# Kernel optimization log

Measured on AMD Instinct MI355X. Metric: run time of the kernel, lower is better.

Reference implementation:

```python
import jax, jax.numpy as jnp
import numpy as np

EMBED_DIM = 1024
NUM_HEADS = 16
HEAD_DIM = EMBED_DIM // NUM_HEADS
B, S = 2, 2048


def setup_inputs() -> dict:
    key = jax.random.key(0)
    ks = jax.random.split(key, 12)
    sd = 1.0 / np.sqrt(EMBED_DIM)
    def lin(kw, kb):
        W = jax.random.uniform(kw, (EMBED_DIM, EMBED_DIM), jnp.float32, -sd, sd)
        b = jax.random.uniform(kb, (EMBED_DIM,), jnp.float32, -sd, sd)
        return W, b
    Wq, bq = lin(ks[0], ks[1])
    Wk, bk = lin(ks[2], ks[3])
    Wv, bv = lin(ks[4], ks[5])
    Wo, bo = lin(ks[6], ks[7])
    q = jax.random.normal(ks[8], (B, S, EMBED_DIM), jnp.float32)
    k = jax.random.normal(ks[9], (B, S, EMBED_DIM), jnp.float32)
    v = jax.random.normal(ks[10], (B, S, EMBED_DIM), jnp.float32)
    # broadcastable causal mask: True = keep (mask==0 positions get -inf)
    attn_mask = jnp.tril(jnp.ones((S, S), jnp.bool_))[None, None]
    return {"q": q, "k": k, "v": v,
            "Wq": Wq, "bq": bq, "Wk": Wk, "bk": bk,
            "Wv": Wv, "bv": bv, "Wo": Wo, "bo": bo,
            "attn_mask": attn_mask}


def reference(q, k, v, Wq, bq, Wk, bk, Wv, bv, Wo, bo, attn_mask):
    bsz, tgt_len, _ = q.shape
    src_len = k.shape[1]
    scale = jnp.sqrt(jnp.float32(HEAD_DIM))
    # projections: PyTorch Linear is x @ W.T + b
    qh = (q @ Wq.T + bq).reshape(bsz, tgt_len, NUM_HEADS, HEAD_DIM).transpose(0, 2, 1, 3)
    kh = (k @ Wk.T + bk).reshape(bsz, src_len, NUM_HEADS, HEAD_DIM).transpose(0, 2, 1, 3)
    vh = (v @ Wv.T + bv).reshape(bsz, src_len, NUM_HEADS, HEAD_DIM).transpose(0, 2, 1, 3)
    # [B,H,T,S] scores
    scores = jnp.einsum('bhtd,bhsd->bhts', qh, kh) / scale
    scores = jnp.where(attn_mask, scores, -jnp.inf)
    attn = jax.nn.softmax(scores, axis=-1)
    out = jnp.einsum('bhts,bhsd->bhtd', attn, vh)  # [B,H,T,D]
    out = out.transpose(0, 2, 1, 3).reshape(bsz, tgt_len, EMBED_DIM)
    return out @ Wo.T + bo
```

## Files before the change

kernel.cpp:

```cpp
#include <hip/hip_runtime.h>
#include <hip/hip_bf16.h>
#include <stdint.h>
#include <stddef.h>

typedef __hip_bfloat16 bf16_t;
typedef __attribute__((ext_vector_type(8))) short short8;
typedef __attribute__((ext_vector_type(4))) short short4v;
typedef __attribute__((ext_vector_type(4))) float floatx4;

#define EMBED 1024
#define NHEAD 16
#define HDIM  64
#define BATCH 2
#define SEQ   2048
#define MTOT  (BATCH*SEQ)
#define NEG_INF (-1e30f)
#define SCALE2 0.18033688011112042f

#define MFMA16(a,b,c) __builtin_amdgcn_mfma_f32_16x16x32_bf16(a,b,c,0,0,0)

static __device__ __forceinline__ short bf16_bits(float x) {
    return __builtin_bit_cast(short, __float2bfloat16(x));
}

static __device__ __forceinline__ float fast_exp2(float x) {
#if __has_builtin(__builtin_amdgcn_exp2f)
    return __builtin_amdgcn_exp2f(x);
#else
    return __expf(x * 0.6931471805599453f);
#endif
}

static __device__ __forceinline__ void async_ld16(const bf16_t* g, short* l) {
    __builtin_amdgcn_global_load_lds(
        (const __attribute__((address_space(1))) void*)g,
        (__attribute__((address_space(3))) void*)l,
        16, 0, 0);
}

static __device__ __forceinline__ void store_out(float* p, float v)  { *p = v; }
static __device__ __forceinline__ void store_out(bf16_t* p, float v) { *p = __float2bfloat16(v); }

__global__ __launch_bounds__(256)
void cvt_all(const float* __restrict__ q, const float* __restrict__ k, const float* __restrict__ v,
             const float* __restrict__ wq, const float* __restrict__ wk,
             const float* __restrict__ wv, const float* __restrict__ wo,
             bf16_t* __restrict__ Qx, bf16_t* __restrict__ Kx, bf16_t* __restrict__ Vx,
             bf16_t* __restrict__ Wqb, bf16_t* __restrict__ Wkb,
             bf16_t* __restrict__ Wvb, bf16_t* __restrict__ Wob)
{
    const float* s; bf16_t* d; int n;
    switch (blockIdx.y) {
        case 0:  s = q;  d = Qx;  n = MTOT * EMBED;  break;
        case 1:  s = k;  d = Kx;  n = MTOT * EMBED;  break;
        case 2:  s = v;  d = Vx;  n = MTOT * EMBED;  break;
        case 3:  s = wq; d = Wqb; n = EMBED * EMBED; break;
        case 4:  s = wk; d = Wkb; n = EMBED * EMBED; break;
        case 5:  s = wv; d = Wvb; n = EMBED * EMBED; break;
        default: s = wo; d = Wob; n = EMBED * EMBED; break;
    }
    const int i4 = (int)blockIdx.x * 256 + (int)threadIdx.x;
    if (i4 * 4 < n) {
        const float4 f = ((const float4*)s)[i4];
        short4v o;
        o[0] = bf16_bits(f.x); o[1] = bf16_bits(f.y);
        o[2] = bf16_bits(f.z); o[3] = bf16_bits(f.w);
        ((short4v*)d)[i4] = o;
    }
}

template <typename OutT, bool VT>
static __device__ __forceinline__ void gemm_tile_128(
    const bf16_t* __restrict__ A, const bf16_t* __restrict__ W,
    const float* __restrict__ bias, OutT* __restrict__ C)
{
    const int N = 1024, K = 1024;
    __shared__ alignas(16) short As[128*32];
    __shared__ alignas(16) short Bs[128*32];

    const int tid  = threadIdx.x;
    const int wave = tid >> 6;
    const int lane = tid & 63;
    const int nbn = N >> 7;
    const int bm = (int)blockIdx.x / nbn;
    const int bn = (int)blockIdx.x % nbn;
    const int m0 = bm << 7, n0 = bn << 7;

    const int wm = ((wave >> 1) & 1) << 6;
    const int wn = (wave & 1) << 6;

    floatx4 acc[4][4] = {};

    const int srow = (wave << 5) + (lane >> 2);
    const int scol = (lane & 3) << 3;
    const bf16_t* gA = A + (size_t)(m0 + srow) * K + scol;
    const bf16_t* gB = W + (size_t)(n0 + srow) * K + scol;
    short* lA0 = &As[(wave << 10)];
    short* lA1 = &As[(wave << 10) + 512];
    short* lB0 = &Bs[(wave << 10)];
    short* lB1 = &Bs[(wave << 10) + 512];

    const int fr = lane & 15;
    const int fk = (lane >> 4) << 3;

    for (int k0 = 0; k0 < K; k0 += 32) {
        __syncthreads();
        async_ld16(gA,                  lA0);
        async_ld16(gA + (size_t)16 * K, lA1);
        async_ld16(gB,                  lB0);
        async_ld16(gB + (size_t)16 * K, lB1);
        gA += 32; gB += 32;
        __syncthreads();

        short8 af[4], bfr[4];
        #pragma unroll
        for (int i = 0; i < 4; ++i)
            af[i] = *(const short8*)&As[(wm + (i << 4) + fr) * 32 + fk];
        #pragma unroll
        for (int j = 0; j < 4; ++j)
            bfr[j] = *(const short8*)&Bs[(wn + (j << 4) + fr) * 32 + fk];
        #pragma unroll
        for (int i = 0; i < 4; ++i)
            #pragma unroll
            for (int j = 0; j < 4; ++j)
                acc[i][j] = MFMA16(af[i], bfr[j], acc[i][j]);
    }

    const int q4 = (lane >> 4) << 2;
    #pragma unroll
    for (int j = 0; j < 4; ++j) {
        const int n = n0 + wn + (j << 4) + fr;
        const float bv = bias[n];
        #pragma unroll
        for (int i = 0; i < 4; ++i) {
            const int mb = m0 + wm + (i << 4) + q4;
            if (VT) {
                const int bb = mb >> 11, ss = mb & 2047;
                short4v pk;
                #pragma unroll
                for (int r = 0; r < 4; ++r)
                    pk[r] = bf16_bits(acc[i][j][r] + bv);
                *(short4v*)((bf16_t*)C + ((size_t)(bb * 1024 + n) << 11) + ss) = pk;
            } else {
                #pragma unroll
                for (int r = 0; r < 4; ++r)
                    store_out(&C[(size_t)(mb + r) * N + n], acc[i][j][r] + bv);
            }
        }
    }
}

__global__ __launch_bounds__(256)
void qkv_proj(const bf16_t* __restrict__ xq, const bf16_t* __restrict__ xk,
              const bf16_t* __restrict__ xv,
              const bf16_t* __restrict__ Wq, const bf16_t* __restrict__ Wk,
              const bf16_t* __restrict__ Wv,
              const float* __restrict__ bq, const float* __restrict__ bk,
              const float* __restrict__ bv,
              bf16_t* __restrict__ Qp, bf16_t* __restrict__ Kp, bf16_t* __restrict__ Vtp)
{
    if (blockIdx.z == 0)      gemm_tile_128<bf16_t, false>(xq, Wq, bq, Qp);
    else if (blockIdx.z == 1) gemm_tile_128<bf16_t, false>(xk, Wk, bk, Kp);
    else                      gemm_tile_128<bf16_t, true >(xv, Wv, bv, Vtp);
}

__global__ __launch_bounds__(256)
void out_proj(const bf16_t* __restrict__ AO, const bf16_t* __restrict__ Wo,
              const float* __restrict__ bo, float* __restrict__ out)
{
    gemm_tile_128<float, false>(AO, Wo, bo, out);
}

__global__ __launch_bounds__(64)
void attn_causal(const bf16_t* __restrict__ Qp, const bf16_t* __restrict__ Kp,
                 const bf16_t* __restrict__ Vt, bf16_t* __restrict__ AO,
                 float* __restrict__ Op, float* __restrict__ Mp, float* __restrict__ Lp)
{
    __shared__ alignas(16) short Pbuf[2][16 * 40];

    const int lane = (int)threadIdx.x & 63;
    const int bid  = (int)blockIdx.x;
    const int bh   = bid & 31;
    const int w    = bid >> 5;
    int tile, sidx, c0, c1;
    bool split;
    if (w < 64) {
        tile  = 63 - (w >> 1);
        sidx  = w & 1;
        split = true;
        const int nch = tile + 1;
        const int h1  = (nch + 1) >> 1;
        c0 = sidx ? h1 : 0;
        c1 = sidx ? nch : h1;
    } else {
        tile  = 95 - w;
        sidx  = 0;
        split = false;
        c0 = 0;
        c1 = tile + 1;
    }
    const bool hasdiag = (c1 == tile + 1);
    const int b = bh >> 4, h = bh & 15;
    const int q0 = tile << 5;

    const int fr   = lane & 15;
    const int quad = lane >> 4;
    const int fk   = quad << 3;

    const bf16_t* Q0 = Qp + (size_t)(b * SEQ + q0 + fr) * EMBED + h * HDIM;
    const short8 aq00 = *(const short8*)(Q0 + fk);
    const short8 aq01 = *(const short8*)(Q0 + 32 + fk);
    const short8 aq10 = *(const short8*)(Q0 + (size_t)16 * EMBED + fk);
    const short8 aq11 = *(const short8*)(Q0 + (size_t)16 * EMBED + 32 + fk);

    const bf16_t* Kbase = Kp + (size_t)(b * SEQ) * EMBED + h * HDIM;
    const bf16_t* Vbase = Vt + ((size_t)(b * 1024 + h * HDIM) << 11);

    floatx4 o0[4] = {}, o1[4] = {};
    float m0 = NEG_INF, m1 = NEG_INF;
    float l0 = 0.f, l1 = 0.f;

    short* Pw0 = &Pbuf[0][0];
    short* Pw1 = &Pbuf[1][0];

    auto smax_vals = [&](const floatx4& sA, const floatx4& sB, float& m_u, float& l_u,
                         floatx4* o_u, const bool diag, const int u16,
                         float* v0, float* v1) {
        float mx = NEG_INF;
        #pragma unroll
        for (int r = 0; r < 4; ++r) {
            float a  = sA[r] * SCALE2;
            float bb = sB[r] * SCALE2;
            if (diag) {
                const int kq = (quad << 2) + r;
                const int lq = u16 + fr;
                if (kq > lq)      a  = NEG_INF;
                if (kq + 16 > lq) bb = NEG_INF;
            }
            v0[r] = a; v1[r] = bb;
            mx = fmaxf(mx, fmaxf(a, bb));
        }
        if (__any(mx > m_u + 8.0f)) {
            mx = fmaxf(mx, __shfl_xor(mx, 16, 64));
            mx = fmaxf(mx, __shfl_xor(mx, 32, 64));
            const float mn = fmaxf(m_u, mx);
            const float al = fast_exp2(m_u - mn);
            m_u = mn;
            l_u *= al;
            #pragma unroll
            for (int r = 0; r < 4; ++r) {
                const float ao = __shfl(al, (lane & 48) | ((quad << 2) + r), 64);
                #pragma unroll
                for (int t = 0; t < 4; ++t) o_u[t][r] *= ao;
            }
        }
        float ls = 0.f;
        #pragma unroll
        for (int r = 0; r < 4; ++r) {
            v0[r] = fast_exp2(v0[r] - m_u);
            v1[r] = fast_exp2(v1[r] - m_u);
            ls += v0[r] + v1[r];
        }
        l_u += ls;
    };

#define KLOAD(K0_, K1_, K2_, K3_, kvo) do {                                  \
        const bf16_t* Kr0_ = Kbase + (size_t)((kvo) + fr) * EMBED;           \
        const bf16_t* Kr1_ = Kr0_ + (size_t)16 * EMBED;                      \
        K0_ = *(const short8*)(Kr0_ + fk);                                   \
        K1_ = *(const short8*)(Kr0_ + 32 + fk);                              \
        K2_ = *(const short8*)(Kr1_ + fk);                                   \
        K3_ = *(const short8*)(Kr1_ + 32 + fk);                              \
    } while (0)

#define ITER(KC0, KC1, KC2, KC3, KN0, KN1, KN2, KN3, DIAGF, PREF) do {       \
        const int kv0 = c << 5;                                              \
           \
        const short8 vf0 = *(const short8*)(Vbase + ((size_t)(fr)      << 11) + kv0 + fk); \
        const short8 vf1 = *(const short8*)(Vbase + ((size_t)(16 + fr) << 11) + kv0 + fk); \
        const short8 vf2 = *(const short8*)(Vbase + ((size_t)(32 + fr) << 11) + kv0 + fk); \
        const short8 vf3 = *(const short8*)(Vbase + ((size_t)(48 + fr) << 11) + kv0 + fk); \
        floatx4 s00 = {}, s01 = {}, s10 = {}, s11 = {};                      \
        s00 = MFMA16(KC0, aq00, s00); s00 = MFMA16(KC1, aq01, s00);          \
        s10 = MFMA16(KC0, aq10, s10); s10 = MFMA16(KC1, aq11, s10);          \
        s01 = MFMA16(KC2, aq00, s01); s01 = MFMA16(KC3, aq01, s01);          \
        s11 = MFMA16(KC2, aq10, s11); s11 = MFMA16(KC3, aq11, s11);          \
        if (PREF) { KLOAD(KN0, KN1, KN2, KN3, kv0 + 32); }                   \
        float p00[4], p01[4], p10[4], p11[4];                                \
        smax_vals(s00, s01, m0, l0, o0, DIAGF, 0,  p00, p01);                \
        smax_vals(s10, s11, m1, l1, o1, DIAGF, 16, p10, p11);                \
        short4v wa0, wa1, wb0, wb1;                                          \
        _Pragma("unroll")                                                    \
        for (int r = 0; r < 4; ++r) {                                        \
            wa0[r] = bf16_bits(p00[r]); wa1[r] = bf16_bits(p01[r]);          \
            wb0[r] = bf16_bits(p10[r]); wb1[r] = bf16_bits(p11[r]);          \
        }                                                                    \
        *(short4v*)&Pw0[fr * 40 + (quad << 2)]      = wa0;                   \
        *(short4v*)&Pw0[fr * 40 + 16 + (quad << 2)] = wa1;                   \
        *(short4v*)&Pw1[fr * 40 + (quad << 2)]      = wb0;                   \
        *(short4v*)&Pw1[fr * 40 + 16 + (quad << 2)] = wb1;                   \
        __asm__ volatile("" ::: "memory");     \
        const short8 pa0 = *(const short8*)&Pw0[fr * 40 + fk];               \
        const short8 pa1 = *(const short8*)&Pw1[fr * 40 + fk];               \
        __asm__ volatile("" ::: "memory");                                   \
        o0[0] = MFMA16(pa0, vf0, o0[0]); o1[0] = MFMA16(pa1, vf0, o1[0]);    \
        o0[1] = MFMA16(pa0, vf1, o0[1]); o1[1] = MFMA16(pa1, vf1, o1[1]);    \
        o0[2] = MFMA16(pa0, vf2, o0[2]); o1[2] = MFMA16(pa1, vf2, o1[2]);    \
        o0[3] = MFMA16(pa0, vf3, o0[3]); o1[3] = MFMA16(pa1, vf3, o1[3]);    \
    } while (0)

    short8 ka0, ka1, ka2, ka3, kb0, kb1, kb2, kb3;
    KLOAD(ka0, ka1, ka2, ka3, c0 << 5);

    int c = c0;
    const int cl = c1 - 1;
    if (cl > c0) {
        for (;;) {
            ITER(ka0, ka1, ka2, ka3, kb0, kb1, kb2, kb3, false, true);
            if (++c == cl) break;
            ITER(kb0, kb1, kb2, kb3, ka0, ka1, ka2, ka3, false, true);
            if (++c == cl) break;
        }
    }
    if ((c - c0) & 1) { ITER(kb0, kb1, kb2, kb3, ka0, ka1, ka2, ka3, hasdiag, false); }
    else              { ITER(ka0, ka1, ka2, ka3, kb0, kb1, kb2, kb3, hasdiag, false); }

#undef ITER
#undef KLOAD

    { float t = __shfl_xor(l0, 16, 64); l0 += t; t = __shfl_xor(l0, 32, 64); l0 += t; }
    { float t = __shfl_xor(l1, 16, 64); l1 += t; t = __shfl_xor(l1, 32, 64); l1 += t; }

    if (!split) {
        const float r0 = 1.0f / l0;
        const float r1 = 1.0f / l1;
        #pragma unroll
        for (int r = 0; r < 4; ++r) {
            const int src = (lane & 48) | ((quad << 2) + r);
            const float i0 = __shfl(r0, src, 64);
            const float i1 = __shfl(r1, src, 64);
            const int row0 = q0 + (quad << 2) + r;
            bf16_t* out0 = AO + (size_t)(b * SEQ + row0) * EMBED + h * HDIM + fr;
            bf16_t* out1 = out0 + (size_t)16 * EMBED;
            #pragma unroll
            for (int t = 0; t < 4; ++t) {
                out0[t << 4] = __float2bfloat16(o0[t][r] * i0);
                out1[t << 4] = __float2bfloat16(o1[t][r] * i1);
            }
        }
    } else {
        const int p = (bh << 5) | (tile - 32);
        float* Ob = Op + (((size_t)sidx << 10) + p) * 2048;
        #pragma unroll
        for (int r = 0; r < 4; ++r) {
            const int row0 = (quad << 2) + r;
            #pragma unroll
            for (int t = 0; t < 4; ++t) {
                Ob[row0 * 64 + (t << 4) + fr]        = o0[t][r];
                Ob[(16 + row0) * 64 + (t << 4) + fr] = o1[t][r];
            }
        }
        if (quad == 0) {
            const size_t mb = (((size_t)sidx << 10) + p) * 32;
            Mp[mb + fr]      = m0;
            Mp[mb + 16 + fr] = m1;
            Lp[mb + fr]      = l0;
            Lp[mb + 16 + fr] = l1;
        }
    }
}

__global__ __launch_bounds__(256)
void attn_combine(const float* __restrict__ Op, const float* __restrict__ Mp,
                  const float* __restrict__ Lp, bf16_t* __restrict__ AO)
{
    const int p   = (int)blockIdx.x;
    const int tid = (int)threadIdx.x;
    const int row = tid >> 3;
    const int d0  = (tid & 7) << 3;
    const int bh = p >> 5, tile = 32 + (p & 31);
    const int b = bh >> 4, h = bh & 15;

    const float m0 = Mp[(size_t)p * 32 + row];
    const float m1 = Mp[(size_t)(1024 + p) * 32 + row];
    const float l0 = Lp[(size_t)p * 32 + row];
    const float l1 = Lp[(size_t)(1024 + p) * 32 + row];
    const float M  = fmaxf(m0, m1);
    const float w0 = fast_exp2(m0 - M);
    const float w1 = fast_exp2(m1 - M);
    const float rd = 1.0f / (l0 * w0 + l1 * w1);

    const float* O0 = Op + ((size_t)p << 11) + row * 64 + d0;
    const float* O1 = O0 + ((size_t)1024 << 11);
    const float4 a0 = *(const float4*)O0;
    const float4 a1 = *(const float4*)(O0 + 4);
    const float4 c0 = *(const float4*)O1;
    const float4 c1 = *(const float4*)(O1 + 4);

    short8 pk;
    pk[0] = bf16_bits((a0.x * w0 + c0.x * w1) * rd);
    pk[1] = bf16_bits((a0.y * w0 + c0.y * w1) * rd);
    pk[2] = bf16_bits((a0.z * w0 + c0.z * w1) * rd);
    pk[3] = bf16_bits((a0.w * w0 + c0.w * w1) * rd);
    pk[4] = bf16_bits((a1.x * w0 + c1.x * w1) * rd);
    pk[5] = bf16_bits((a1.y * w0 + c1.y * w1) * rd);
    pk[6] = bf16_bits((a1.z * w0 + c1.z * w1) * rd);
    pk[7] = bf16_bits((a1.w * w0 + c1.w * w1) * rd);
    *(short8*)(AO + (size_t)(b * SEQ + tile * 32 + row) * EMBED + h * HDIM + d0) = pk;
}

extern "C" void kernel_launch(void* const* d_in, const int* in_sizes, int n_in,
                              void* d_out, int out_size, void* d_ws, size_t ws_size,
                              hipStream_t stream)
{
    (void)in_sizes; (void)n_in; (void)out_size; (void)ws_size;
    const float* q  = (const float*)d_in[0];
    const float* k  = (const float*)d_in[1];
    const float* v  = (const float*)d_in[2];
    const float* Wq = (const float*)d_in[3];
    const float* bq = (const float*)d_in[4];
    const float* Wk = (const float*)d_in[5];
    const float* bk = (const float*)d_in[6];
    const float* Wv = (const float*)d_in[7];
    const float* bv = (const float*)d_in[8];
    const float* Wo = (const float*)d_in[9];
    const float* bo = (const float*)d_in[10];

    const size_t NX = (size_t)MTOT * EMBED;
    const size_t NW = (size_t)EMBED * EMBED;
    bf16_t* Qx  = (bf16_t*)d_ws;
    bf16_t* Kx  = Qx  + NX;
    bf16_t* Vx  = Kx  + NX;
    bf16_t* Wqb = Vx  + NX;
    bf16_t* Wkb = Wqb + NW;
    bf16_t* Wvb = Wkb + NW;
    bf16_t* Wob = Wvb + NW;
    bf16_t* Qp  = Wob + NW;
    bf16_t* Kp  = Qp  + NX;
    bf16_t* Vtp = Kp  + NX;
    bf16_t* AO  = Vtp + NX;

    float* Op = (float*)Qx;
    float* Mp = (float*)Wqb;
    float* Lp = Mp + 2 * 1024 * 32;

    dim3 blk(256);
    cvt_all<<<dim3(4096, 7), blk, 0, stream>>>(q, k, v, Wq, Wk, Wv, Wo,
                                               Qx, Kx, Vx, Wqb, Wkb, Wvb, Wob);
    qkv_proj<<<dim3(256, 1, 3), blk, 0, stream>>>(Qx, Kx, Vx, Wqb, Wkb, Wvb,
                                                  bq, bk, bv, Qp, Kp, Vtp);
    attn_causal<<<dim3(3072), dim3(64), 0, stream>>>(Qp, Kp, Vtp, AO, Op, Mp, Lp);
    attn_combine<<<dim3(1024), blk, 0, stream>>>(Op, Mp, Lp, AO);
    out_proj<<<dim3(256), blk, 0, stream>>>(AO, Wob, bo, (float*)d_out);
}
```

Before: 286.7 us.

## Keep attention P in registers via permlane swaps, fold scale into Q projection

The attention kernel stops staging the probability tile through LDS and instead builds the P operand with bf16 packing and permlane32/16 swaps. It swaps the MFMA operand order so the output accumulators are transposed, which allows vectorized output stores and per-lane rescaling without shuffles. The softmax scale is folded into the Q projection epilogue, and the K prefetch is issued earlier. The output projection uses a 64-row tile so it launches twice as many blocks. The permlane path depends on gfx950 instruction support and on the transposed fragment layout being correct.

```diff
diff --git a/kernel.cpp b/kernel.cpp
--- a/kernel.cpp
+++ b/kernel.cpp
@@ -7,6 +7,8 @@
 typedef __attribute__((ext_vector_type(8))) short short8;
 typedef __attribute__((ext_vector_type(4))) short short4v;
 typedef __attribute__((ext_vector_type(4))) float floatx4;
+typedef __attribute__((ext_vector_type(4))) unsigned uint4v;
+typedef __attribute__((ext_vector_type(2))) unsigned uint2v;
 
 #define EMBED 1024
 #define NHEAD 16
@@ -28,6 +30,29 @@
     return __builtin_amdgcn_exp2f(x);
 #else
     return __expf(x * 0.6931471805599453f);
+#endif
+}
+
+static __device__ __forceinline__ unsigned pack_bf16x2(float lo, float hi) {
+    const unsigned a = (unsigned)(unsigned short)bf16_bits(lo);
+    const unsigned b = (unsigned)(unsigned short)bf16_bits(hi);
+    return a | (b << 16);
+}
+
+static __device__ __forceinline__ void permswap32(unsigned& a, unsigned& b) {
+#if __has_builtin(__builtin_amdgcn_permlane32_swap)
+    uint2v r = __builtin_amdgcn_permlane32_swap(a, b, false, false);
+    a = r[0]; b = r[1];
+#else
+    asm volatile("v_permlane32_swap_b32 %0, %1" : "+v"(a), "+v"(b));
+#endif
+}
+static __device__ __forceinline__ void permswap16(unsigned& a, unsigned& b) {
+#if __has_builtin(__builtin_amdgcn_permlane16_swap)
+    uint2v r = __builtin_amdgcn_permlane16_swap(a, b, false, false);
+    a = r[0]; b = r[1];
+#else
+    asm volatile("v_permlane16_swap_b32 %0, %1" : "+v"(a), "+v"(b));
 #endif
 }
 
@@ -69,58 +94,60 @@
     }
 }
 
-template <typename OutT, bool VT>
-static __device__ __forceinline__ void gemm_tile_128(
+template <typename OutT, bool VT, int BM>
+static __device__ __forceinline__ void gemm_tile(
     const bf16_t* __restrict__ A, const bf16_t* __restrict__ W,
-    const float* __restrict__ bias, OutT* __restrict__ C)
-{
+    const float* __restrict__ bias, OutT* __restrict__ C, const float scale)
+{
+    constexpr int MI = BM >> 5;
+    constexpr int RPW = BM >> 2;
     const int N = 1024, K = 1024;
-    __shared__ alignas(16) short As[128*32];
-    __shared__ alignas(16) short Bs[128*32];
+    __shared__ alignas(16) short As[BM * 32];
+    __shared__ alignas(16) short Bs[128 * 32];
 
     const int tid  = threadIdx.x;
     const int wave = tid >> 6;
     const int lane = tid & 63;
-    const int nbn = N >> 7;
-    const int bm = (int)blockIdx.x / nbn;
-    const int bn = (int)blockIdx.x % nbn;
-    const int m0 = bm << 7, n0 = bn << 7;
-
-    const int wm = ((wave >> 1) & 1) << 6;
+    const int bm = (int)blockIdx.x >> 3;
+    const int bn = (int)blockIdx.x & 7;
+    const int m0 = bm * BM, n0 = bn << 7;
+
+    const int wm = ((wave >> 1) & 1) * (BM >> 1);
     const int wn = (wave & 1) << 6;
 
-    floatx4 acc[4][4] = {};
-
-    const int srow = (wave << 5) + (lane >> 2);
-    const int scol = (lane & 3) << 3;
-    const bf16_t* gA = A + (size_t)(m0 + srow) * K + scol;
-    const bf16_t* gB = W + (size_t)(n0 + srow) * K + scol;
-    short* lA0 = &As[(wave << 10)];
-    short* lA1 = &As[(wave << 10) + 512];
+    floatx4 acc[MI][4] = {};
+
+    const int srowA = wave * RPW + (lane >> 2);
+    const int srowB = (wave << 5) + (lane >> 2);
+    const int scol  = (lane & 3) << 3;
+    const bf16_t* gA = A + (size_t)(m0 + srowA) * K + scol;
+    const bf16_t* gB = W + (size_t)(n0 + srowB) * K + scol;
+    short* lA0 = &As[wave * RPW * 32];
+    short* lA1 = lA0 + 512;
     short* lB0 = &Bs[(wave << 10)];
-    short* lB1 = &Bs[(wave << 10) + 512];
+    short* lB1 = lB0 + 512;
 
     const int fr = lane & 15;
     const int fk = (lane >> 4) << 3;
 
     for (int k0 = 0; k0 < K; k0 += 32) {
         __syncthreads();
-        async_ld16(gA,                  lA0);
-        async_ld16(gA + (size_t)16 * K, lA1);
-        async_ld16(gB,                  lB0);
+        async_ld16(gA, lA0);
+        if constexpr (BM == 128) async_ld16(gA + (size_t)16 * K, lA1);
+        async_ld16(gB, lB0);
         async_ld16(gB + (size_t)16 * K, lB1);
         gA += 32; gB += 32;
         __syncthreads();
 
-        short8 af[4], bfr[4];
-        #pragma unroll
-        for (int i = 0; i < 4; ++i)
+        short8 af[MI], bfr[4];
+        #pragma unroll
+        for (int i = 0; i < MI; ++i)
             af[i] = *(const short8*)&As[(wm + (i << 4) + fr) * 32 + fk];
         #pragma unroll
         for (int j = 0; j < 4; ++j)
             bfr[j] = *(const short8*)&Bs[(wn + (j << 4) + fr) * 32 + fk];
         #pragma unroll
-        for (int i = 0; i < 4; ++i)
+        for (int i = 0; i < MI; ++i)
             #pragma unroll
             for (int j = 0; j < 4; ++j)
                 acc[i][j] = MFMA16(af[i], bfr[j], acc[i][j]);
@@ -132,19 +159,19 @@
         const int n = n0 + wn + (j << 4) + fr;
         const float bv = bias[n];
         #pragma unroll
-        for (int i = 0; i < 4; ++i) {
+        for (int i = 0; i < MI; ++i) {
             const int mb = m0 + wm + (i << 4) + q4;
             if (VT) {
                 const int bb = mb >> 11, ss = mb & 2047;
                 short4v pk;
                 #pragma unroll
                 for (int r = 0; r < 4; ++r)
-                    pk[r] = bf16_bits(acc[i][j][r] + bv);
+                    pk[r] = bf16_bits((acc[i][j][r] + bv) * scale);
                 *(short4v*)((bf16_t*)C + ((size_t)(bb * 1024 + n) << 11) + ss) = pk;
             } else {
                 #pragma unroll
                 for (int r = 0; r < 4; ++r)
-                    store_out(&C[(size_t)(mb + r) * N + n], acc[i][j][r] + bv);
+                    store_out(&C[(size_t)(mb + r) * N + n], (acc[i][j][r] + bv) * scale);
             }
         }
     }
@@ -159,16 +186,16 @@
               const float* __restrict__ bv,
               bf16_t* __restrict__ Qp, bf16_t* __restrict__ Kp, bf16_t* __restrict__ Vtp)
 {
-    if (blockIdx.z == 0)      gemm_tile_128<bf16_t, false>(xq, Wq, bq, Qp);
-    else if (blockIdx.z == 1) gemm_tile_128<bf16_t, false>(xk, Wk, bk, Kp);
-    else                      gemm_tile_128<bf16_t, true >(xv, Wv, bv, Vtp);
+    if (blockIdx.z == 0)      gemm_tile<bf16_t, false, 128>(xq, Wq, bq, Qp, SCALE2);
+    else if (blockIdx.z == 1) gemm_tile<bf16_t, false, 128>(xk, Wk, bk, Kp, 1.0f);
+    else                      gemm_tile<bf16_t, true , 128>(xv, Wv, bv, Vtp, 1.0f);
 }
 
 __global__ __launch_bounds__(256)
 void out_proj(const bf16_t* __restrict__ AO, const bf16_t* __restrict__ Wo,
               const float* __restrict__ bo, float* __restrict__ out)
 {
-    gemm_tile_128<float, false>(AO, Wo, bo, out);
+    gemm_tile<float, false, 64>(AO, Wo, bo, out, 1.0f);
 }
 
 __global__ __launch_bounds__(64)
@@ -176,8 +203,6 @@
                  const bf16_t* __restrict__ Vt, bf16_t* __restrict__ AO,
                  float* __restrict__ Op, float* __restrict__ Mp, float* __restrict__ Lp)
 {
-    __shared__ alignas(16) short Pbuf[2][16 * 40];
-
     const int lane = (int)threadIdx.x & 63;
     const int bid  = (int)blockIdx.x;
     const int bh   = bid & 31;
@@ -220,17 +245,13 @@
     float m0 = NEG_INF, m1 = NEG_INF;
     float l0 = 0.f, l1 = 0.f;
 
-    short* Pw0 = &Pbuf[0][0];
-    short* Pw1 = &Pbuf[1][0];
-
-    auto smax_vals = [&](const floatx4& sA, const floatx4& sB, float& m_u, float& l_u,
-                         floatx4* o_u, const bool diag, const int u16,
-                         float* v0, float* v1) {
-        float mx = NEG_INF;
+    auto smax_pb = [&](const floatx4& sA, const floatx4& sB, float& m_u, float& l_u,
+                       floatx4* o_u, const bool diag, const int u16) -> short8 {
+        float v0[4], v1[4];
         #pragma unroll
         for (int r = 0; r < 4; ++r) {
-            float a  = sA[r] * SCALE2;
-            float bb = sB[r] * SCALE2;
+            float a  = sA[r];
+            float bb = sB[r];
             if (diag) {
                 const int kq = (quad << 2) + r;
                 const int lq = u16 + fr;
@@ -238,8 +259,9 @@
                 if (kq + 16 > lq) bb = NEG_INF;
             }
             v0[r] = a; v1[r] = bb;
-            mx = fmaxf(mx, fmaxf(a, bb));
-        }
+        }
+        float mx = fmaxf(fmaxf(fmaxf(v0[0], v0[1]), fmaxf(v0[2], v0[3])),
+                         fmaxf(fmaxf(v1[0], v1[1]), fmaxf(v1[2], v1[3])));
         if (__any(mx > m_u + 8.0f)) {
             mx = fmaxf(mx, __shfl_xor(mx, 16, 64));
             mx = fmaxf(mx, __shfl_xor(mx, 32, 64));
@@ -248,11 +270,9 @@
             m_u = mn;
             l_u *= al;
             #pragma unroll
-            for (int r = 0; r < 4; ++r) {
-                const float ao = __shfl(al, (lane & 48) | ((quad << 2) + r), 64);
+            for (int t = 0; t < 4; ++t)
                 #pragma unroll
-                for (int t = 0; t < 4; ++t) o_u[t][r] *= ao;
-            }
+                for (int r = 0; r < 4; ++r) o_u[t][r] *= al;
         }
         float ls = 0.f;
         #pragma unroll
@@ -262,6 +282,16 @@
             ls += v0[r] + v1[r];
         }
         l_u += ls;
+        unsigned c0p = pack_bf16x2(v0[0], v0[1]);
+        unsigned c1p = pack_bf16x2(v0[2], v0[3]);
+        unsigned d0p = pack_bf16x2(v1[0], v1[1]);
+        unsigned d1p = pack_bf16x2(v1[2], v1[3]);
+        permswap32(c0p, d0p);
+        permswap32(c1p, d1p);
+        permswap16(c0p, d0p);
+        permswap16(c1p, d1p);
+        uint4v wv; wv[0] = c0p; wv[1] = c1p; wv[2] = d0p; wv[3] = d1p;
+        return __builtin_bit_cast(short8, wv);
     };
 
 #define KLOAD(K0_, K1_, K2_, K3_, kvo) do {                                  \
@@ -275,38 +305,23 @@
 
 #define ITER(KC0, KC1, KC2, KC3, KN0, KN1, KN2, KN3, DIAGF, PREF) do {       \
         const int kv0 = c << 5;                                              \
-           \
+         \
         const short8 vf0 = *(const short8*)(Vbase + ((size_t)(fr)      << 11) + kv0 + fk); \
         const short8 vf1 = *(const short8*)(Vbase + ((size_t)(16 + fr) << 11) + kv0 + fk); \
         const short8 vf2 = *(const short8*)(Vbase + ((size_t)(32 + fr) << 11) + kv0 + fk); \
         const short8 vf3 = *(const short8*)(Vbase + ((size_t)(48 + fr) << 11) + kv0 + fk); \
+        if (PREF) { KLOAD(KN0, KN1, KN2, KN3, kv0 + 32); }                   \
         floatx4 s00 = {}, s01 = {}, s10 = {}, s11 = {};                      \
         s00 = MFMA16(KC0, aq00, s00); s00 = MFMA16(KC1, aq01, s00);          \
         s10 = MFMA16(KC0, aq10, s10); s10 = MFMA16(KC1, aq11, s10);          \
         s01 = MFMA16(KC2, aq00, s01); s01 = MFMA16(KC3, aq01, s01);          \
         s11 = MFMA16(KC2, aq10, s11); s11 = MFMA16(KC3, aq11, s11);          \
-        if (PREF) { KLOAD(KN0, KN1, KN2, KN3, kv0 + 32); }                   \
-        float p00[4], p01[4], p10[4], p11[4];                                \
-        smax_vals(s00, s01, m0, l0, o0, DIAGF, 0,  p00, p01);                \
-        smax_vals(s10, s11, m1, l1, o1, DIAGF, 16, p10, p11);                \
-        short4v wa0, wa1, wb0, wb1;                                          \
-        _Pragma("unroll")                                                    \
-        for (int r = 0; r < 4; ++r) {                                        \
-            wa0[r] = bf16_bits(p00[r]); wa1[r] = bf16_bits(p01[r]);          \
-            wb0[r] = bf16_bits(p10[r]); wb1[r] = bf16_bits(p11[r]);          \
-        }                                                                    \
-        *(short4v*)&Pw0[fr * 40 + (quad << 2)]      = wa0;                   \
-        *(short4v*)&Pw0[fr * 40 + 16 + (quad << 2)] = wa1;                   \
-        *(short4v*)&Pw1[fr * 40 + (quad << 2)]      = wb0;                   \
-        *(short4v*)&Pw1[fr * 40 + 16 + (quad << 2)] = wb1;                   \
-        __asm__ volatile("" ::: "memory");     \
-        const short8 pa0 = *(const short8*)&Pw0[fr * 40 + fk];               \
-        const short8 pa1 = *(const short8*)&Pw1[fr * 40 + fk];               \
-        __asm__ volatile("" ::: "memory");                                   \
-        o0[0] = MFMA16(pa0, vf0, o0[0]); o1[0] = MFMA16(pa1, vf0, o1[0]);    \
-        o0[1] = MFMA16(pa0, vf1, o0[1]); o1[1] = MFMA16(pa1, vf1, o1[1]);    \
-        o0[2] = MFMA16(pa0, vf2, o0[2]); o1[2] = MFMA16(pa1, vf2, o1[2]);    \
-        o0[3] = MFMA16(pa0, vf3, o0[3]); o1[3] = MFMA16(pa1, vf3, o1[3]);    \
+        const short8 pb0 = smax_pb(s00, s01, m0, l0, o0, DIAGF, 0);          \
+        const short8 pb1 = smax_pb(s10, s11, m1, l1, o1, DIAGF, 16);         \
+        o0[0] = MFMA16(vf0, pb0, o0[0]); o1[0] = MFMA16(vf0, pb1, o1[0]);    \
+        o0[1] = MFMA16(vf1, pb0, o0[1]); o1[1] = MFMA16(vf1, pb1, o1[1]);    \
+        o0[2] = MFMA16(vf2, pb0, o0[2]); o1[2] = MFMA16(vf2, pb1, o1[2]);    \
+        o0[3] = MFMA16(vf3, pb0, o0[3]); o1[3] = MFMA16(vf3, pb1, o1[3]);    \
     } while (0)
 
     short8 ka0, ka1, ka2, ka3, kb0, kb1, kb2, kb3;
@@ -332,33 +347,28 @@
     { float t = __shfl_xor(l1, 16, 64); l1 += t; t = __shfl_xor(l1, 32, 64); l1 += t; }
 
     if (!split) {
-        const float r0 = 1.0f / l0;
-        const float r1 = 1.0f / l1;
-        #pragma unroll
-        for (int r = 0; r < 4; ++r) {
-            const int src = (lane & 48) | ((quad << 2) + r);
-            const float i0 = __shfl(r0, src, 64);
-            const float i1 = __shfl(r1, src, 64);
-            const int row0 = q0 + (quad << 2) + r;
-            bf16_t* out0 = AO + (size_t)(b * SEQ + row0) * EMBED + h * HDIM + fr;
-            bf16_t* out1 = out0 + (size_t)16 * EMBED;
+        const float i0 = 1.0f / l0;
+        const float i1 = 1.0f / l1;
+        bf16_t* out0 = AO + (size_t)(b * SEQ + q0 + fr) * EMBED + h * HDIM + (quad << 2);
+        bf16_t* out1 = out0 + (size_t)16 * EMBED;
+        #pragma unroll
+        for (int t = 0; t < 4; ++t) {
+            short4v pk0, pk1;
             #pragma unroll
-            for (int t = 0; t < 4; ++t) {
-                out0[t << 4] = __float2bfloat16(o0[t][r] * i0);
-                out1[t << 4] = __float2bfloat16(o1[t][r] * i1);
+            for (int r = 0; r < 4; ++r) {
+                pk0[r] = bf16_bits(o0[t][r] * i0);
+                pk1[r] = bf16_bits(o1[t][r] * i1);
             }
+            *(short4v*)(out0 + (t << 4)) = pk0;
+            *(short4v*)(out1 + (t << 4)) = pk1;
         }
     } else {
         const int p = (bh << 5) | (tile - 32);
         float* Ob = Op + (((size_t)sidx << 10) + p) * 2048;
         #pragma unroll
-        for (int r = 0; r < 4; ++r) {
-            const int row0 = (quad << 2) + r;
-            #pragma unroll
-            for (int t = 0; t < 4; ++t) {
-                Ob[row0 * 64 + (t << 4) + fr]        = o0[t][r];
-                Ob[(16 + row0) * 64 + (t << 4) + fr] = o1[t][r];
-            }
+        for (int t = 0; t < 4; ++t) {
+            *(floatx4*)&Ob[fr * 64 + (t << 4) + (quad << 2)]        = o0[t];
+            *(floatx4*)&Ob[(16 + fr) * 64 + (t << 4) + (quad << 2)] = o1[t];
         }
         if (quad == 0) {
             const size_t mb = (((size_t)sidx << 10) + p) * 32;
@@ -451,5 +461,5 @@
                                                   bq, bk, bv, Qp, Kp, Vtp);
     attn_causal<<<dim3(3072), dim3(64), 0, stream>>>(Qp, Kp, Vtp, AO, Op, Mp, Lp);
     attn_combine<<<dim3(1024), blk, 0, stream>>>(Op, Mp, Lp, AO);
-    out_proj<<<dim3(256), blk, 0, stream>>>(AO, Wob, bo, (float*)d_out);
-}
+    out_proj<<<dim3(512), blk, 0, stream>>>(AO, Wob, bo, (float*)d_out);
+}
```

Result: no change. 284.1 us (-0.9%).
